# Kernel optimization log

Hardware: AMD Instinct MI355X
Metric: run time of the kernel (lower is better)

## Reference

```python
import jax, jax.numpy as jnp
import numpy as np

N = 16384      # points
C = 512        # channels (d_model)
D_INNER = 1024 # expand=2
D_STATE = 16
D_CONV = 4
DT_RANK = 32   # ceil(C/16)
MLP = 1024     # mlp_ratio=2
EPS = 1e-5


def setup_inputs() -> dict:
    key = jax.random.key(0)
    ks = jax.random.split(key, 16)
    s = 0.02
    feat = jax.random.normal(ks[0], (N, C), jnp.float32)
    perm = np.random.RandomState(0).permutation(N)
    order = jnp.asarray(perm, jnp.int32)
    inverse = jnp.asarray(np.argsort(perm), jnp.int32)
    inp = dict(
        feat=feat, order=order, inverse=inverse,
        ln1_w=jnp.ones((C,)), ln1_b=jnp.zeros((C,)),
        in_proj_w=s * jax.random.normal(ks[1], (2 * D_INNER, C)),
        conv_w=s * jax.random.normal(ks[2], (D_INNER, D_CONV)),
        conv_b=jnp.zeros((D_INNER,)),
        x_proj_w=s * jax.random.normal(ks[3], (DT_RANK + 2 * D_STATE, D_INNER)),
        dt_proj_w=s * jax.random.normal(ks[4], (D_INNER, DT_RANK)),
        dt_proj_b=jnp.full((D_INNER,), -2.0),  # softplus(-2) ~ small dt, like mamba init
        A_log=jnp.log(jnp.tile(jnp.arange(1, D_STATE + 1, dtype=jnp.float32)[None, :], (D_INNER, 1))),
        D_skip=jnp.ones((D_INNER,)),
        out_proj_w=s * jax.random.normal(ks[5], (C, D_INNER)),
        ln2_w=jnp.ones((C,)), ln2_b=jnp.zeros((C,)),
        ffn_w1=s * jax.random.normal(ks[6], (C, MLP)), ffn_b1=jnp.zeros((MLP,)),
        ffn_w2=s * jax.random.normal(ks[7], (MLP, C)), ffn_b2=jnp.zeros((C,)),
    )
    return inp


def _layer_norm(x, w, b):
    mu = jnp.mean(x, axis=-1, keepdims=True)
    var = jnp.mean(jnp.square(x - mu), axis=-1, keepdims=True)
    return (x - mu) * jax.lax.rsqrt(var + EPS) * w + b


def _mamba(x, in_proj_w, conv_w, conv_b, x_proj_w, dt_proj_w, dt_proj_b,
           A_log, D_skip, out_proj_w):
    # x: (L, C)
    L = x.shape[0]
    xz = x @ in_proj_w.T                      # (L, 2*D_INNER)
    xm, z = jnp.split(xz, 2, axis=-1)
    # depthwise causal conv1d, kernel D_CONV
    xp = jnp.pad(xm, ((D_CONV - 1, 0), (0, 0)))
    xc = conv_b + sum(xp[k:k + L] * conv_w[:, k] for k in range(D_CONV))
    xc = jax.nn.silu(xc)                      # (L, D_INNER)
    dbc = xc @ x_proj_w.T                     # (L, DT_RANK + 2*D_STATE)
    dt, Bm, Cm = jnp.split(dbc, [DT_RANK, DT_RANK + D_STATE], axis=-1)
    dt = jax.nn.softplus(dt @ dt_proj_w.T + dt_proj_b)  # (L, D_INNER)
    A = -jnp.exp(A_log)                       # (D_INNER, D_STATE)

    def step(h, inp):
        dt_t, B_t, C_t, x_t = inp             # (D_INNER,), (D_STATE,), (D_STATE,), (D_INNER,)
        dA = jnp.exp(dt_t[:, None] * A)       # (D_INNER, D_STATE)
        h = dA * h + (dt_t * x_t)[:, None] * B_t[None, :]
        return h, h @ C_t                     # y_t: (D_INNER,)

    h0 = jnp.zeros((D_INNER, D_STATE), xm.dtype)
    _, ys = jax.lax.scan(step, h0, (dt, Bm, Cm, xc))
    y = (ys + xc * D_skip) * jax.nn.silu(z)
    return y @ out_proj_w.T                   # (L, C)


def reference(feat, order, inverse, ln1_w, ln1_b, in_proj_w, conv_w, conv_b,
              x_proj_w, dt_proj_w, dt_proj_b, A_log, D_skip, out_proj_w,
              ln2_w, ln2_b, ffn_w1, ffn_b1, ffn_w2, ffn_b2):
    f = feat[order]                           # gather by serialized order
    x = f + _mamba(_layer_norm(f, ln1_w, ln1_b), in_proj_w, conv_w, conv_b,
                   x_proj_w, dt_proj_w, dt_proj_b, A_log, D_skip, out_proj_w)
    h = _layer_norm(x, ln2_w, ln2_b)
    x = x + (jax.nn.gelu(h @ ffn_w1 + ffn_b1, approximate=False) @ ffn_w2 + ffn_b2)
    return x[inverse]                         # scatter back to original order
```

## Files before the change

kernel.cpp:

```cpp
#include <hip/hip_runtime.h>


#define DEV __device__ __forceinline__

typedef unsigned short u16;
typedef u16    u16x8  __attribute__((ext_vector_type(8)));
typedef __bf16 bf16x8 __attribute__((ext_vector_type(8)));
typedef float  f32x4  __attribute__((ext_vector_type(4)));

static constexpr int L_SEQ = 16384;
static constexpr int LC    = 64;
static constexpr int NCH   = 256;

DEV u16 f2b(float x){
  union { float f; unsigned u; } c; c.f = x;
  unsigned u = c.u;
  return (u16)((u + 0x7fffu + ((u >> 16) & 1u)) >> 16);
}
DEV float b2f(u16 h){
  union { unsigned u; float f; } c; c.u = ((unsigned)h) << 16;
  return c.f;
}
DEV int ldix(const void* p, int l, bool is64){
  return is64 ? (int)((const long long*)p)[l] : ((const int*)p)[l];
}
DEV float siluf(float x){ return x / (1.f + __expf(-x)); }
DEV float softplusf(float x){
  return fmaxf(x, 0.f) + __logf(1.f + __expf(-fabsf(x)));
}
DEV float geluf(float x){ return 0.5f * x * (1.f + erff(x * 0.70710678118f)); }

DEV void gld_lds16(const u16* g, u16* l){
  __builtin_amdgcn_global_load_lds(
      (const __attribute__((address_space(1))) unsigned*)g,
      (__attribute__((address_space(3))) unsigned*)l, 16, 0, 0);
}

DEV void pow16(float r, float* a){
  float r2 = r * r, r4 = r2 * r2, r8 = r4 * r4;
  a[0] = r;        a[1] = r2;       a[2] = r2 * r;    a[3] = r4;
  a[4] = r4 * r;   a[5] = r4 * r2;  a[6] = r4 * a[2]; a[7] = r8;
  a[8] = r8 * r;   a[9] = r8 * r2;  a[10] = r8 * a[2]; a[11] = r8 * r4;
  a[12] = r8 * a[4]; a[13] = r8 * a[5]; a[14] = r8 * a[6]; a[15] = r8 * r8;
}

__global__ __launch_bounds__(256) void fill_k(float* out, float v, unsigned n){
  unsigned i = blockIdx.x * 256 + threadIdx.x;
  if (i < n) out[i] = v;
}

__global__ void detect_k(const int* ord32, int* flag){
  flag[0] = (ord32[1] == 0 && ord32[3] == 0 && ord32[5] == 0) ? 1 : 0;
  flag[1] = 0;
}

__global__ __launch_bounds__(256) void checkA_k(const float* __restrict__ alog,
                                                int* flag){
  int i = blockIdx.x * 256 + threadIdx.x;
  int s = i & 15;
  float v = alog[i];
  float base = alog[i - s];
  if (fabsf(v - (base + __logf((float)(s + 1)))) > 1e-4f) atomicOr(flag + 1, 1);
}

struct NT4 { const float* src[4]; unsigned off[5]; };
__global__ __launch_bounds__(256) void normw_k(NT4 t, u16* dst){
  unsigned i = blockIdx.x * 256 + threadIdx.x;
  if (i >= t.off[4]) return;
  int s = 0;
  #pragma unroll
  for (int k = 1; k <= 3; k++) s += (i >= t.off[k]) ? 1 : 0;
  dst[i] = f2b(t.src[s][i - t.off[s]]);
}

__global__ __launch_bounds__(256) void convT_kernel(const float* __restrict__ in,
                                                    u16* __restrict__ out, int K, int N){
  __shared__ float t[32][33];
  int k0 = blockIdx.x * 32, n0 = blockIdx.y * 32;
  int tx = threadIdx.x & 31, ty = threadIdx.x >> 5;
  #pragma unroll
  for (int i = 0; i < 32; i += 8)
    t[ty + i][tx] = in[(size_t)(k0 + ty + i) * N + n0 + tx];
  __syncthreads();
  #pragma unroll
  for (int i = 0; i < 32; i += 8)
    out[(size_t)(n0 + ty + i) * K + k0 + tx] = f2b(t[tx][ty + i]);
}

__global__ __launch_bounds__(256) void gather_ln1(const float* __restrict__ feat,
    const void* order, const float* __restrict__ w, const float* __restrict__ b,
    const int* flag, u16* __restrict__ x1b){
  __shared__ float rs_[256], rq_[256];
  const bool is64 = flag[0] != 0;
  int l = blockIdx.x, tid = threadIdx.x;
  int src = ldix(order, l, is64);
  float v0 = feat[(size_t)src * 512 + tid];
  float v1 = feat[(size_t)src * 512 + tid + 256];
  rs_[tid] = v0 + v1; rq_[tid] = v0 * v0 + v1 * v1;
  __syncthreads();
  for (int o = 128; o; o >>= 1){
    if (tid < o){ rs_[tid] += rs_[tid + o]; rq_[tid] += rq_[tid + o]; }
    __syncthreads();
  }
  float mu = rs_[0] * (1.f / 512.f);
  float var = rq_[0] * (1.f / 512.f) - mu * mu;
  float rstd = rsqrtf(var + 1e-5f);
  x1b[(size_t)l * 512 + tid]       = f2b((v0 - mu) * rstd * w[tid]       + b[tid]);
  x1b[(size_t)l * 512 + tid + 256] = f2b((v1 - mu) * rstd * w[tid + 256] + b[tid + 256]);
}

__global__ __launch_bounds__(256) void ln2_kernel(const float* __restrict__ x,
    const float* __restrict__ w, const float* __restrict__ b, u16* __restrict__ h2b){
  __shared__ float rs_[256], rq_[256];
  int l = blockIdx.x, tid = threadIdx.x;
  float v0 = x[(size_t)l * 512 + tid];
  float v1 = x[(size_t)l * 512 + tid + 256];
  rs_[tid] = v0 + v1; rq_[tid] = v0 * v0 + v1 * v1;
  __syncthreads();
  for (int o = 128; o; o >>= 1){
    if (tid < o){ rs_[tid] += rs_[tid + o]; rq_[tid] += rq_[tid + o]; }
    __syncthreads();
  }
  float mu = rs_[0] * (1.f / 512.f);
  float var = rq_[0] * (1.f / 512.f) - mu * mu;
  float rstd = rsqrtf(var + 1e-5f);
  h2b[(size_t)l * 512 + tid]       = f2b((v0 - mu) * rstd * w[tid]       + b[tid]);
  h2b[(size_t)l * 512 + tid + 256] = f2b((v1 - mu) * rstd * w[tid + 256] + b[tid + 256]);
}

__global__ __launch_bounds__(256) void conv_silu(const u16* __restrict__ xm,
    const float* __restrict__ cw, const float* __restrict__ cb, u16* __restrict__ xcb){
  constexpr int TT = 8;
  const int tid = threadIdx.x;
  const int d0 = (tid & 127) * 8;
  const int t0 = (blockIdx.x * 2 + (tid >> 7)) * TT;

  float wk[4][8], bias[8];
  #pragma unroll
  for (int j = 0; j < 8; j++) bias[j] = cb[d0 + j];
  #pragma unroll
  for (int j = 0; j < 8; j++){
    f32x4 v = *(const f32x4*)(cw + (d0 + j) * 4);
    wk[0][j] = v[0]; wk[1][j] = v[1]; wk[2][j] = v[2]; wk[3][j] = v[3];
  }

  float win[3][8];
  #pragma unroll
  for (int k = 0; k < 3; k++){
    int tt = t0 - 3 + k;
    if (tt >= 0){
      u16x8 v = *(const u16x8*)(xm + (size_t)tt * 1024 + d0);
      #pragma unroll
      for (int j = 0; j < 8; j++) win[k][j] = b2f(v[j]);
    } else {
      #pragma unroll
      for (int j = 0; j < 8; j++) win[k][j] = 0.f;
    }
  }

  #pragma unroll
  for (int t = 0; t < TT; t++){
    u16x8 v = *(const u16x8*)(xm + (size_t)(t0 + t) * 1024 + d0);
    u16x8 o;
    float cu[8];
    #pragma unroll
    for (int j = 0; j < 8; j++){
      cu[j] = b2f(v[j]);
      float acc = bias[j] + win[0][j] * wk[0][j] + win[1][j] * wk[1][j]
                + win[2][j] * wk[2][j] + cu[j] * wk[3][j];
      o[j] = f2b(siluf(acc));
    }
    *(u16x8*)(xcb + (size_t)(t0 + t) * 1024 + d0) = o;
    #pragma unroll
    for (int j = 0; j < 8; j++){
      win[0][j] = win[1][j]; win[1][j] = win[2][j]; win[2][j] = cu[j];
    }
  }
}

enum { M_BF16 = 0, M_INPROJ = 1, M_DT = 2, M_RES = 3, M_GELU = 4, M_FFN2 = 5 };

template<int MODE>
DEV void gemm_epilogue(float v, int m, int n, int N,
    float* __restrict__ outf, u16* __restrict__ outb, u16* __restrict__ outb2,
    const float* __restrict__ auxf, const float* __restrict__ auxw,
    const void* ordv, bool is64){
  size_t o = (size_t)m * N + n;
  if constexpr (MODE == M_BF16){
    outb[o] = f2b(v);
  } else if constexpr (MODE == M_INPROJ){
    if (n < 1024) outb [(size_t)m * 1024 + n]          = f2b(v);
    else          outb2[(size_t)m * 1024 + (n - 1024)] = f2b(siluf(v));
  } else if constexpr (MODE == M_DT){
    outb[o] = f2b(softplusf(v + auxw[n]));
  } else if constexpr (MODE == M_RES){
    int src = ldix(ordv, m, is64);
    outf[o] = v + auxw[(size_t)src * 512 + n];
  } else if constexpr (MODE == M_GELU){
    outb[o] = f2b(geluf(v + auxw[n]));
  } else {
    outf[o] = v + auxw[n] + auxf[o];
  }
}

template<int BM, int BN, int WM, int WN, int MODE>
__global__ __launch_bounds__((BM / WM) * (BN / WN) * 64) void gemm_p2(
    const u16* __restrict__ A, const u16* __restrict__ B,
    int N, int K, int lda, int ldb,
    float* __restrict__ outf, u16* __restrict__ outb, u16* __restrict__ outb2,
    const float* __restrict__ auxf, const float* __restrict__ auxw,
    const void* ordv, const int* flag){
  constexpr int BK = 32;
  constexpr int MI = WM / 16, NI = WN / 16;
  constexpr int WCOLS = BN / WN;
  constexpr int THREADS = (BM / WM) * (BN / WN) * 64;
  constexpr int NA = BM * BK / (THREADS * 8);
  constexpr int NB = BN * BK / (THREADS * 8);
  constexpr int LPS = NA + NB;
  static_assert(LPS == 2 || LPS == 3 || LPS == 4, "vmcnt literals");
  __shared__ __align__(16) u16 sA[3][BM * BK];
  __shared__ __align__(16) u16 sB[3][BN * BK];
  const int tid  = threadIdx.x;
  const int wave = tid >> 6, lane = tid & 63;
  const int wr = wave / WCOLS, wc = wave % WCOLS;
  const int m0 = blockIdx.x * BM, n0 = blockIdx.y * BN;
  const int rr = lane & 15;
  const int qc = lane >> 4;

  f32x4 acc[MI][NI] = {};

  auto stage = [&](int buf, int k0){
    #pragma unroll
    for (int i = 0; i < NA; i++){
      int idx = tid + i * THREADS;
      int row = idx >> 2, sub = idx & 3;
      int cg = (sub - (row >> 1)) & 3;
      gld_lds16(A + (size_t)(m0 + row) * lda + k0 + cg * 8, &sA[buf][idx * 8]);
    }
    #pragma unroll
    for (int i = 0; i < NB; i++){
      int idx = tid + i * THREADS;
      int row = idx >> 2, sub = idx & 3;
      int cg = (sub - (row >> 1)) & 3;
      gld_lds16(B + (size_t)(n0 + row) * ldb + k0 + cg * 8, &sB[buf][idx * 8]);
    }
  };

  const int nst = K / BK;
  stage(0, 0);
  if (nst > 1) stage(1, BK);
  for (int st = 0; st < nst; st++){
    if (st + 2 < nst) stage((st + 2) % 3, (st + 2) * BK);
    const int nf = (st + 2 < nst) ? 2 : ((st + 1 < nst) ? 1 : 0);
    if (nf == 2){
      if constexpr (LPS == 4)      asm volatile("s_waitcnt vmcnt(8)" ::: "memory");
      else if constexpr (LPS == 3) asm volatile("s_waitcnt vmcnt(6)" ::: "memory");
      else                         asm volatile("s_waitcnt vmcnt(4)" ::: "memory");
    } else if (nf == 1){
      if constexpr (LPS == 4)      asm volatile("s_waitcnt vmcnt(4)" ::: "memory");
      else if constexpr (LPS == 3) asm volatile("s_waitcnt vmcnt(3)" ::: "memory");
      else                         asm volatile("s_waitcnt vmcnt(2)" ::: "memory");
    } else {
      asm volatile("s_waitcnt vmcnt(0)" ::: "memory");
    }
    __builtin_amdgcn_s_barrier();
    __builtin_amdgcn_sched_barrier(0);

    const int cur = st % 3;
    bf16x8 af[MI], bfr[NI];
    #pragma unroll
    for (int i = 0; i < MI; i++){
      int R = wr * WM + i * 16 + rr;
      int slot = (qc + (R >> 1)) & 3;
      af[i] = *(const bf16x8*)(&sA[cur][R * BK + slot * 8]);
    }
    #pragma unroll
    for (int j = 0; j < NI; j++){
      int R = wc * WN + j * 16 + rr;
      int slot = (qc + (R >> 1)) & 3;
      bfr[j] = *(const bf16x8*)(&sB[cur][R * BK + slot * 8]);
    }
    #pragma unroll
    for (int i = 0; i < MI; i++)
      #pragma unroll
      for (int j = 0; j < NI; j++)
        acc[i][j] = __builtin_amdgcn_mfma_f32_16x16x32_bf16(af[i], bfr[j], acc[i][j], 0, 0, 0);

    asm volatile("s_waitcnt lgkmcnt(0)" ::: "memory");
    __builtin_amdgcn_s_barrier();
    __builtin_amdgcn_sched_barrier(0);
  }

  const bool is64 = flag ? (flag[0] != 0) : false;
  #pragma unroll
  for (int i = 0; i < MI; i++)
    #pragma unroll
    for (int j = 0; j < NI; j++)
      #pragma unroll
      for (int r = 0; r < 4; r++){
        int m = m0 + wr * WM + i * 16 + ((lane >> 4) << 2) + r;
        int n = n0 + wc * WN + j * 16 + (lane & 15);
        gemm_epilogue<MODE>(acc[i][j][r], m, n, N, outf, outb, outb2,
                            auxf, auxw, ordv, is64);
      }
}

template<int BM, int BN, int WM, int WN, int MODE>
__global__ __launch_bounds__(256) void gemm_bt(
    const u16* __restrict__ A, const u16* __restrict__ B,
    int N, int K, int lda, int ldb,
    float* __restrict__ outf, u16* __restrict__ outb, u16* __restrict__ outb2,
    const float* __restrict__ auxf, const float* __restrict__ auxw,
    const void* ordv, const int* flag){
  constexpr int BK = 32;
  constexpr int MI = WM / 16, NI = WN / 16;
  constexpr int WCOLS = BN / WN;
  constexpr int NA = BM * 4 / 256;
  constexpr int NB = BN * 4 / 256;
  __shared__ __align__(16) u16 sA[BM * BK];
  __shared__ __align__(16) u16 sB[BN * BK];
  const int tid  = threadIdx.x;
  const int wave = tid >> 6, lane = tid & 63;
  const int wr = wave / WCOLS, wc = wave % WCOLS;
  const int m0 = blockIdx.x * BM, n0 = blockIdx.y * BN;
  const int rr = lane & 15;
  const int qk = (lane >> 4) * 8;

  f32x4 acc[MI][NI] = {};

  for (int k0 = 0; k0 < K; k0 += BK){
    #pragma unroll
    for (int i = 0; i < NA; i++){
      int idx = tid + i * 256;
      int r = idx >> 2, c = (idx & 3) * 8;
      gld_lds16(A + (size_t)(m0 + r) * lda + k0 + c, sA + (size_t)idx * 8);
    }
    #pragma unroll
    for (int i = 0; i < NB; i++){
      int idx = tid + i * 256;
      int r = idx >> 2, c = (idx & 3) * 8;
      gld_lds16(B + (size_t)(n0 + r) * ldb + k0 + c, sB + (size_t)idx * 8);
    }
    __syncthreads();

    bf16x8 af[MI], bfr[NI];
    #pragma unroll
    for (int i = 0; i < MI; i++)
      af[i] = *(const bf16x8*)(sA + (wr * WM + i * 16 + rr) * BK + qk);
    #pragma unroll
    for (int j = 0; j < NI; j++)
      bfr[j] = *(const bf16x8*)(sB + (wc * WN + j * 16 + rr) * BK + qk);
    #pragma unroll
    for (int i = 0; i < MI; i++)
      #pragma unroll
      for (int j = 0; j < NI; j++)
        acc[i][j] = __builtin_amdgcn_mfma_f32_16x16x32_bf16(af[i], bfr[j], acc[i][j], 0, 0, 0);
    __syncthreads();
  }

  const bool is64 = flag ? (flag[0] != 0) : false;
  #pragma unroll
  for (int i = 0; i < MI; i++)
    #pragma unroll
    for (int j = 0; j < NI; j++)
      #pragma unroll
      for (int r = 0; r < 4; r++){
        int m = m0 + wr * WM + i * 16 + ((lane >> 4) << 2) + r;
        int n = n0 + wc * WN + j * 16 + (lane & 15);
        gemm_epilogue<MODE>(acc[i][j][r], m, n, N, outf, outb, outb2,
                            auxf, auxw, ordv, is64);
      }
}

__global__ __launch_bounds__(256) void scan_pass1(const u16* __restrict__ dt,
    const u16* __restrict__ xc, const u16* __restrict__ dbc,
    const float* __restrict__ alog, const int* __restrict__ flag,
    u16* __restrict__ chP, u16* __restrict__ chH){
  __shared__ float sB[LC * 16];
  const int chunk = blockIdx.x;
  const int d = blockIdx.y * 256 + threadIdx.x;
  const int t0 = chunk * LC;
  for (int i = threadIdx.x; i < LC * 16; i += 256){
    int t = i >> 4, s = i & 15;
    sB[i] = b2f(dbc[(size_t)(t0 + t) * 64 + 32 + s]);
  }
  __syncthreads();
  float h[16];
  #pragma unroll
  for (int s = 0; s < 16; s++) h[s] = 0.f;
  float P[16];
  const bool fastA = (flag[1] == 0);
  if (fastA){
    const float a0 = -__expf(alog[(size_t)d * 16]);
    float R = 1.f;
    for (int t = 0; t < LC; t++){
      float dtv = b2f(dt[(size_t)(t0 + t) * 1024 + d]);
      float xv  = b2f(xc[(size_t)(t0 + t) * 1024 + d]);
      float dtx = dtv * xv;
      float r = __expf(dtv * a0);
      R *= r;
      float a_[16];
      pow16(r, a_);
      #pragma unroll
      for (int s = 0; s < 16; s++)
        h[s] = a_[s] * h[s] + dtx * sB[t * 16 + s];
    }
    pow16(R, P);
  } else {
    float A[16];
    #pragma unroll
    for (int s = 0; s < 16; s++){
      A[s] = -__expf(alog[(size_t)d * 16 + s]);
      P[s] = 1.f;
    }
    for (int t = 0; t < LC; t++){
      float dtv = b2f(dt[(size_t)(t0 + t) * 1024 + d]);
      float xv  = b2f(xc[(size_t)(t0 + t) * 1024 + d]);
      float dtx = dtv * xv;
      #pragma unroll
      for (int s = 0; s < 16; s++){
        float a = __expf(dtv * A[s]);
        P[s] *= a;
        h[s] = a * h[s] + dtx * sB[t * 16 + s];
      }
    }
  }
  #pragma unroll
  for (int s = 0; s < 16; s++){
    chP[((size_t)chunk * 16 + s) * 1024 + d] = f2b(P[s]);
    chH[((size_t)chunk * 16 + s) * 1024 + d] = f2b(h[s]);
  }
}

__global__ __launch_bounds__(64) void carry_scan(const u16* chP, const u16* chH,
                                                 u16* hin){
  int id = blockIdx.x * 64 + threadIdx.x;
  float h = 0.f;
  for (int k = 0; k < NCH; k += 8){
    float P[8], E[8];
    #pragma unroll
    for (int j = 0; j < 8; j++){
      P[j] = b2f(chP[(size_t)(k + j) * 16384 + id]);
      E[j] = b2f(chH[(size_t)(k + j) * 16384 + id]);
    }
    #pragma unroll
    for (int j = 0; j < 8; j++){
      hin[(size_t)(k + j) * 16384 + id] = f2b(h);
      h = P[j] * h + E[j];
    }
  }
}

__global__ __launch_bounds__(256) void scan_pass3(const u16* __restrict__ dt,
    const u16* xc, const u16* __restrict__ dbc,
    const float* __restrict__ alog, const int* __restrict__ flag,
    const u16* __restrict__ hin,
    const float* __restrict__ dskip, const u16* __restrict__ zsil, u16* yb){
  __shared__ float sBC[LC * 32];
  const int chunk = blockIdx.x;
  const int d = blockIdx.y * 256 + threadIdx.x;
  const int t0 = chunk * LC;
  for (int i = threadIdx.x; i < LC * 32; i += 256){
    int t = i >> 5, c = i & 31;
    sBC[i] = b2f(dbc[(size_t)(t0 + t) * 64 + 32 + c]);
  }
  __syncthreads();
  float h[16];
  #pragma unroll
  for (int s = 0; s < 16; s++)
    h[s] = b2f(hin[((size_t)chunk * 16 + s) * 1024 + d]);
  const float Dv = dskip[d];
  const bool fastA = (flag[1] == 0);
  if (fastA){
    const float a0 = -__expf(alog[(size_t)d * 16]);
    for (int t = 0; t < LC; t++){
      float dtv = b2f(dt[(size_t)(t0 + t) * 1024 + d]);
      float xv  = b2f(xc[(size_t)(t0 + t) * 1024 + d]);
      float dtx = dtv * xv;
      float r = __expf(dtv * a0);
      float a_[16];
      pow16(r, a_);
      float y = 0.f;
      #pragma unroll
      for (int s = 0; s < 16; s++){
        h[s] = a_[s] * h[s] + dtx * sBC[t * 32 + s];
        y += h[s] * sBC[t * 32 + 16 + s];
      }
      float rv = (y + xv * Dv) * b2f(zsil[(size_t)(t0 + t) * 1024 + d]);
      yb[(size_t)(t0 + t) * 1024 + d] = f2b(rv);
    }
  } else {
    float A[16];
    #pragma unroll
    for (int s = 0; s < 16; s++) A[s] = -__expf(alog[(size_t)d * 16 + s]);
    for (int t = 0; t < LC; t++){
      float dtv = b2f(dt[(size_t)(t0 + t) * 1024 + d]);
      float xv  = b2f(xc[(size_t)(t0 + t) * 1024 + d]);
      float dtx = dtv * xv;
      float y = 0.f;
      #pragma unroll
      for (int s = 0; s < 16; s++){
        float a = __expf(dtv * A[s]);
        h[s] = a * h[s] + dtx * sBC[t * 32 + s];
        y += h[s] * sBC[t * 32 + 16 + s];
      }
      float rv = (y + xv * Dv) * b2f(zsil[(size_t)(t0 + t) * 1024 + d]);
      yb[(size_t)(t0 + t) * 1024 + d] = f2b(rv);
    }
  }
}

__global__ __launch_bounds__(256) void final_gather(const float* __restrict__ xfin,
    const void* inv, const int* flag, float* __restrict__ out){
  const bool is64 = flag[0] != 0;
  int i = blockIdx.x, tid = threadIdx.x;
  int src = ldix(inv, i, is64);
  out[(size_t)i * 512 + tid]       = xfin[(size_t)src * 512 + tid];
  out[(size_t)i * 512 + tid + 256] = xfin[(size_t)src * 512 + tid + 256];
}

extern "C" void kernel_launch(void* const* d_in, const int* in_sizes, int n_in,
                              void* d_out, int out_size, void* d_ws, size_t ws_size,
                              hipStream_t stream){
  float* out = (float*)d_out;
  char* w = (char*)d_ws;

  constexpr size_t OFF_W1T  = 3342336;
  constexpr size_t OFF_W2T  = OFF_W1T + 1048576;
  constexpr size_t OFF_FLAG = OFF_W2T + 1048576;
  constexpr size_t OFF_XMB  = 5439744;
  constexpr size_t OFF_ZSIL = OFF_XMB  + 33554432;
  constexpr size_t OFF_XCB  = OFF_ZSIL + 33554432;
  constexpr size_t OFF_X1B  = OFF_XCB  + 33554432;
  constexpr size_t OFF_DBC  = OFF_X1B  + 16777216;
  constexpr size_t OFF_CHP  = OFF_X1B;
  constexpr size_t OFF_CHH  = OFF_X1B  + 8388608;
  constexpr size_t WS_NEED  = OFF_DBC  + 2097152;

  int code = 0;
  static const int want[20] = {8388608,16384,16384,512,512,1048576,4096,1024,
                               65536,32768,1024,16384,1024,524288,512,512,
                               524288,1024,524288,512};
  if (n_in != 20) code = 1000;
  else {
    for (int i = 0; i < 20 && !code; i++)
      if (in_sizes[i] != want[i]) code = 2000 + i * 50;
    if (!code && out_size != 8388608) code = 3000;
    if (!code && ws_size < WS_NEED)   code = 4000;
  }
  if (code){
    unsigned n = (unsigned)(out_size > 0 ? out_size : 1);
    fill_k<<<(n + 255) / 256, 256, 0, stream>>>(out, (float)code, n);
    return;
  }

  u16*   w1tb = (u16*)(w + OFF_W1T);
  u16*   w2tb = (u16*)(w + OFF_W2T);
  int*   flag = (int*)(w + OFF_FLAG);
  u16*   xmb  = (u16*)(w + OFF_XMB);
  u16*   zsil = (u16*)(w + OFF_ZSIL);
  u16*   xcb  = (u16*)(w + OFF_XCB);
  u16*   x1b  = (u16*)(w + OFF_X1B);
  u16*   dbcb = (u16*)(w + OFF_DBC);
  u16*   chP  = (u16*)(w + OFF_CHP);
  u16*   chH  = (u16*)(w + OFF_CHH);
  float* x    = (float*)(w + OFF_XMB);
  float* xfin = (float*)(w + OFF_XCB);
  u16* dtb  = xmb;
  u16* yb   = xcb;
  u16* midb = zsil;
  u16* h2b  = x1b;
  u16* hin  = chP;

  u16* nb = (u16*)w;
  u16* inpjn  = nb;
  u16* xpjn   = nb + 1048576;
  u16* dtpjn  = nb + 1114112;
  u16* outpjn = nb + 1146880;
  NT4 t;
  t.src[0] = (const float*)d_in[5];  t.src[1] = (const float*)d_in[8];
  t.src[2] = (const float*)d_in[9];  t.src[3] = (const float*)d_in[13];
  t.off[0] = 0; t.off[1] = 1048576; t.off[2] = 1114112; t.off[3] = 1146880; t.off[4] = 1671168;

  detect_k<<<1, 1, 0, stream>>>((const int*)d_in[1], flag);
  checkA_k<<<64, 256, 0, stream>>>((const float*)d_in[11], flag);
  normw_k<<<(1671168 + 255) / 256, 256, 0, stream>>>(t, nb);
  convT_kernel<<<dim3(16, 32), 256, 0, stream>>>((const float*)d_in[16], w1tb, 512, 1024);
  convT_kernel<<<dim3(32, 16), 256, 0, stream>>>((const float*)d_in[18], w2tb, 1024, 512);

  gather_ln1<<<L_SEQ, 256, 0, stream>>>((const float*)d_in[0], d_in[1],
      (const float*)d_in[3], (const float*)d_in[4], flag, x1b);

  gemm_p2<256,128,64,64,M_INPROJ><<<dim3(64,16),512,0,stream>>>(
      x1b, inpjn, 2048, 512, 512, 512, nullptr, xmb, zsil, nullptr, nullptr, nullptr, nullptr);

  conv_silu<<<1024, 256, 0, stream>>>(xmb,
      (const float*)d_in[6], (const float*)d_in[7], xcb);

  gemm_p2<64,64,16,64,M_BF16><<<dim3(256,1),256,0,stream>>>(
      xcb, xpjn, 64, 1024, 1024, 1024, nullptr, dbcb, nullptr, nullptr, nullptr, nullptr, nullptr);

  gemm_bt<128,128,64,64,M_DT><<<dim3(128,8),256,0,stream>>>(
      dbcb, dtpjn, 1024, 32, 64, 32, nullptr, dtb, nullptr, nullptr,
      (const float*)d_in[10], nullptr, nullptr);

  scan_pass1<<<dim3(NCH,4),256,0,stream>>>(dtb, xcb, dbcb,
      (const float*)d_in[11], flag, chP, chH);
  carry_scan<<<256,64,0,stream>>>(chP, chH, hin);
  scan_pass3<<<dim3(NCH,4),256,0,stream>>>(dtb, xcb, dbcb,
      (const float*)d_in[11], flag, hin, (const float*)d_in[12], zsil, yb);

  gemm_p2<256,128,64,64,M_RES><<<dim3(64,4),512,0,stream>>>(
      yb, outpjn, 512, 1024, 1024, 1024, x, nullptr, nullptr, nullptr,
      (const float*)d_in[0], d_in[1], flag);

  ln2_kernel<<<L_SEQ,256,0,stream>>>(x, (const float*)d_in[14], (const float*)d_in[15], h2b);

  gemm_p2<256,128,64,64,M_GELU><<<dim3(64,8),512,0,stream>>>(
      h2b, w1tb, 1024, 512, 512, 512, nullptr, midb, nullptr, nullptr,
      (const float*)d_in[17], nullptr, nullptr);

  gemm_p2<256,128,64,64,M_FFN2><<<dim3(64,4),512,0,stream>>>(
      midb, w2tb, 512, 1024, 1024, 1024, xfin, nullptr, nullptr, x,
      (const float*)d_in[19], nullptr, nullptr);

  final_gather<<<L_SEQ,256,0,stream>>>(xfin, d_in[2], flag, out);
}
```

Measured before the change: 492.2 us.

## Add 256x256 eight-phase pipelined GEMM for in_proj and FFN1

Adds a new GEMM kernel with 256x256 block tiles and BK=64. It double-buffers LDS with XOR-swizzled direct global-to-LDS loads and splits each K-step pair into eight phases that interleave MFMA bursts (under raised s_setprio) with staged prefetches and explicit vmcnt waits. It replaces the 256x128 gemm_p2 for the in_proj and FFN1 GEMMs, aiming to raise arithmetic intensity and overlap memory with MFMA. The trade-offs are 128KB of LDS per block, which limits occupancy, and many barriers per phase.

Result: slower. 504.5 us (+2.5%).

```diff
diff --git a/kernel.cpp b/kernel.cpp
--- a/kernel.cpp
+++ b/kernel.cpp
@@ -201,6 +201,112 @@
   } else {
     outf[o] = v + auxw[n] + auxf[o];
   }
+}
+
+#define PH8(BUF, MH, KS, LOADB, ...)                                        \
+  do {                                                                      \
+    bf16x8 af_[4];                                                          \
+    _Pragma("unroll")                                                       \
+    for (int mi = 0; mi < 4; mi++){                                         \
+      int R = wr * 128 + (MH) * 64 + mi * 16 + rr;                          \
+      int slot = ((KS) * 4 + qc) ^ (R & 7);                                 \
+      af_[mi] = *(const bf16x8*)(&sA[BUF][R * 64 + slot * 8]);              \
+    }                                                                       \
+    if constexpr (LOADB){                                                   \
+      _Pragma("unroll")                                                     \
+      for (int nj = 0; nj < 4; nj++){                                       \
+        int R = wc * 64 + nj * 16 + rr;                                     \
+        int slot = ((KS) * 4 + qc) ^ (R & 7);                               \
+        bfr[KS][nj] = *(const bf16x8*)(&sB[BUF][R * 64 + slot * 8]);        \
+      }                                                                     \
+    }                                                                       \
+    __VA_ARGS__;                                                            \
+    __builtin_amdgcn_s_barrier();                                           \
+    asm volatile("s_waitcnt lgkmcnt(0)" ::: "memory");                      \
+    __builtin_amdgcn_sched_barrier(0);                                      \
+    __builtin_amdgcn_s_setprio(1);                                          \
+    _Pragma("unroll")                                                       \
+    for (int mi = 0; mi < 4; mi++)                                          \
+      _Pragma("unroll")                                                     \
+      for (int nj = 0; nj < 4; nj++)                                        \
+        acc[(MH) * 4 + mi][nj] = __builtin_amdgcn_mfma_f32_16x16x32_bf16(   \
+            af_[mi], bfr[KS][nj], acc[(MH) * 4 + mi][nj], 0, 0, 0);         \
+    __builtin_amdgcn_s_setprio(0);                                          \
+    __builtin_amdgcn_s_barrier();                                           \
+  } while (0)
+
+template<int MODE>
+__global__ __launch_bounds__(512, 2) void gemm_8ph(
+    const u16* __restrict__ A, const u16* __restrict__ B,
+    int N, int K, int lda, int ldb,
+    float* __restrict__ outf, u16* __restrict__ outb, u16* __restrict__ outb2,
+    const float* __restrict__ auxf, const float* __restrict__ auxw,
+    const void* ordv, const int* flag){
+  __shared__ __align__(16) u16 sA[2][256 * 64];
+  __shared__ __align__(16) u16 sB[2][256 * 64];
+  const int tid  = threadIdx.x;
+  const int wave = tid >> 6, lane = tid & 63;
+  const int wr = wave >> 2, wc = wave & 3;
+  const int m0 = blockIdx.x * 256, n0 = blockIdx.y * 256;
+  const int rr = lane & 15, qc = lane >> 4;
+
+  f32x4  acc[8][4] = {};
+  bf16x8 bfr[2][4];
+
+  const int srow = tid >> 3, ssub = tid & 7;
+  auto stA = [&](int buf, int band, int kt){
+    int row = band * 64 + srow;
+    int cg = ssub ^ (row & 7);
+    gld_lds16(A + (size_t)(m0 + row) * lda + kt * 64 + cg * 8,
+              &sA[buf][band * 4096 + tid * 8]);
+  };
+  auto stB = [&](int buf, int band, int kt){
+    int row = band * 64 + srow;
+    int cg = ssub ^ (row & 7);
+    gld_lds16(B + (size_t)(n0 + row) * ldb + kt * 64 + cg * 8,
+              &sB[buf][band * 4096 + tid * 8]);
+  };
+
+  const int nst = K / 64, its = nst / 2;
+
+  stA(0,0,0); stA(0,1,0); stA(0,2,0); stA(0,3,0);
+  stB(0,0,0); stB(0,1,0); stB(0,2,0); stB(0,3,0);
+  stB(1,0,1); stB(1,1,1); stB(1,2,1); stB(1,3,1);
+  stA(1,0,1); stA(1,2,1);
+  asm volatile("s_waitcnt vmcnt(6)" ::: "memory");
+  __builtin_amdgcn_s_barrier();
+
+  for (int it = 0; it < its; ++it){
+    const int k2  = 2 * it + 1;
+    const int kn1 = 2 * it + 2, kn2 = 2 * it + 3;
+    const bool pre = (it + 1 < its);
+    PH8(0, 0, 0, true,  stA(1,1,k2); stA(1,3,k2) );
+    PH8(0, 0, 1, true,  ((void)0) );
+    PH8(0, 1, 0, false, if (pre){ stB(0,0,kn1); stB(0,1,kn1); } );
+    PH8(0, 1, 1, false,
+        if (pre){ stB(0,2,kn1); stB(0,3,kn1); stA(0,0,kn1);
+                  asm volatile("s_waitcnt vmcnt(5)" ::: "memory"); }
+        else    { asm volatile("s_waitcnt vmcnt(0)" ::: "memory"); } );
+    PH8(1, 0, 0, true,  if (pre){ stA(0,2,kn1); stA(0,1,kn1); stA(0,3,kn1); } );
+    PH8(1, 0, 1, true,  ((void)0) );
+    PH8(1, 1, 0, false, if (pre){ stB(1,0,kn2); stB(1,1,kn2); stB(1,2,kn2); } );
+    PH8(1, 1, 1, false,
+        if (pre){ stB(1,3,kn2); stA(1,0,kn2); stA(1,2,kn2);
+                  asm volatile("s_waitcnt vmcnt(6)" ::: "memory"); } );
+  }
+
+  const bool is64 = flag ? (flag[0] != 0) : false;
+  #pragma unroll
+  for (int mi = 0; mi < 8; mi++)
+    #pragma unroll
+    for (int nj = 0; nj < 4; nj++)
+      #pragma unroll
+      for (int r = 0; r < 4; r++){
+        int m = m0 + wr * 128 + mi * 16 + ((lane >> 4) << 2) + r;
+        int n = n0 + wc * 64 + nj * 16 + (lane & 15);
+        gemm_epilogue<MODE>(acc[mi][nj][r], m, n, N, outf, outb, outb2,
+                            auxf, auxw, ordv, is64);
+      }
 }
 
 template<int BM, int BN, int WM, int WN, int MODE>
@@ -591,7 +697,7 @@
   gather_ln1<<<L_SEQ, 256, 0, stream>>>((const float*)d_in[0], d_in[1],
       (const float*)d_in[3], (const float*)d_in[4], flag, x1b);
 
-  gemm_p2<256,128,64,64,M_INPROJ><<<dim3(64,16),512,0,stream>>>(
+  gemm_8ph<M_INPROJ><<<dim3(64,8),512,0,stream>>>(
       x1b, inpjn, 2048, 512, 512, 512, nullptr, xmb, zsil, nullptr, nullptr, nullptr, nullptr);
 
   conv_silu<<<1024, 256, 0, stream>>>(xmb,
@@ -616,7 +722,7 @@
 
   ln2_kernel<<<L_SEQ,256,0,stream>>>(x, (const float*)d_in[14], (const float*)d_in[15], h2b);
 
-  gemm_p2<256,128,64,64,M_GELU><<<dim3(64,8),512,0,stream>>>(
+  gemm_8ph<M_GELU><<<dim3(64,4),512,0,stream>>>(
       h2b, w1tb, 1024, 512, 512, 512, nullptr, midb, nullptr, nullptr,
       (const float*)d_in[17], nullptr, nullptr);
 
```
